# Kernel tuning notes

Hardware: AMD Instinct MI355X
Metric: run time of the kernel (lower is better)

Reference implementation:

```python
import jax, jax.numpy as jnp
import numpy as np
from jax.scipy.special import logsumexp

B, S, H, T, M = 64, 512, 768, 500, 8
POSITION_WEIGHT = 0.6
LABEL_SMOOTH = 0.1
GAMMA = 2.0


def setup_inputs() -> dict:
    key = jax.random.key(0)
    ks = jax.random.split(key, 12)
    hidden = jax.random.normal(ks[0], (B, S, H), jnp.float32)  # BERT sequence_output stand-in
    lengths = jax.random.randint(ks[1], (B,), S // 2, S + 1)
    attention_mask = (jnp.arange(S)[None, :] < lengths[:, None]).astype(jnp.int32)
    position_labels = jax.random.randint(ks[2], (B, S), 0, 3).astype(jnp.int32)
    type_labels = jax.random.randint(ks[3], (B, M), 0, T).astype(jnp.int32)
    starts = jax.random.randint(ks[4], (B, M), 1, S // 2)
    ends = starts + jax.random.randint(ks[5], (B, M), 2, 8)
    valid = jax.random.uniform(ks[6], (B, M)) < 0.8  # some (batch, span) slots unused, like the original sum()>0 filter
    target_positions = jnp.where(valid[..., None], jnp.stack([starts, ends], -1), 0).astype(jnp.int32)
    # CRF params exactly as hardcoded in __init__
    trans = jnp.array([[-5.0, 20.0, -10000.0], [-50.0, 0.0, 50.0], [0.0, -50.0, 30.0]], jnp.float32)
    start_trans = jnp.array([0.0, 0.0, -10000.0], jnp.float32)
    end_trans = jnp.array([0.0, -100.0, 0.0], jnp.float32)
    return {
        'hidden': hidden,
        'attention_mask': attention_mask,
        'position_labels': position_labels,
        'type_labels': type_labels,
        'target_positions': target_positions,
        'bi_label_weight': jnp.asarray(0.5, jnp.float32),
        'W_pos': 0.02 * jax.random.normal(ks[7], (H, 3), jnp.float32),
        'b_pos': jnp.zeros((3,), jnp.float32),
        'start_trans': start_trans,
        'end_trans': end_trans,
        'trans': trans,
        'att_W1': 0.02 * jax.random.normal(ks[8], (H, 64), jnp.float32),
        'att_b1': jnp.zeros((64,), jnp.float32),
        'att_W2': 0.02 * jax.random.normal(ks[9], (64, 1), jnp.float32),
        'att_b2': jnp.zeros((1,), jnp.float32),
        'W_type': 0.02 * jax.random.normal(ks[10], (H, T), jnp.float32),
        'b_type': jnp.zeros((T,), jnp.float32),
    }


def crf_nll(em, labels, mask, start_trans, end_trans, trans):
    # torchcrf-style masked negative log-likelihood, reduction='none'
    maskf = mask.astype(em.dtype)
    emit = jnp.take_along_axis(em, labels[..., None], -1)[..., 0]  # [B,S]
    emit_score = (emit * maskf).sum(1)
    tr = trans[labels[:, :-1], labels[:, 1:]]  # [B,S-1]
    tr_score = (tr * maskf[:, 1:]).sum(1)
    last = mask.sum(1) - 1
    last_tags = jnp.take_along_axis(labels, last[:, None], 1)[:, 0]
    score = start_trans[labels[:, 0]] + emit_score + tr_score + end_trans[last_tags]
    # log partition via scan over time
    alpha = start_trans[None, :] + em[:, 0]  # [B,3]
    def step(alpha, xs):
        em_t, m_t = xs
        nxt = logsumexp(alpha[:, :, None] + trans[None, :, :] + em_t[:, None, :], axis=1)
        return jnp.where(m_t[:, None], nxt, alpha), None
    alpha, _ = jax.lax.scan(step, alpha, (em[:, 1:].transpose(1, 0, 2), mask[:, 1:].T))
    logZ = logsumexp(alpha + end_trans[None, :], axis=-1)
    return logZ - score  # = -log_likelihood


def reference(hidden, attention_mask, position_labels, type_labels, target_positions,
              bi_label_weight, W_pos, b_pos, start_trans, end_trans, trans,
              att_W1, att_b1, att_W2, att_b2, W_type, b_type):
    mask = attention_mask.astype(bool)
    emissions = hidden @ W_pos + b_pos  # [B,S,3]
    w = jnp.where(position_labels > 0, 1.0 + bi_label_weight, 1.0)[..., None]
    em_w = emissions * w
    position_loss = crf_nll(em_w, position_labels, mask, start_trans, end_trans, trans).mean()

    # span attention pooling, batched over all (B,M) pairs instead of the Python loop
    scores = (jnp.tanh(hidden @ att_W1 + att_b1) @ att_W2 + att_b2)[..., 0]  # [B,S]
    starts = target_positions[..., 0]
    ends = target_positions[..., 1]
    valid = target_positions.sum(-1) > 0  # [B,M]
    pos = jnp.arange(hidden.shape[1])
    span_mask = (pos[None, None, :] >= starts[..., None]) & (pos[None, None, :] < ends[..., None])  # [B,M,S]
    att = jnp.where(span_mask, scores[:, None, :], -1e9)
    aw = jax.nn.softmax(att, axis=-1)  # per-span softmax == softmax over the gathered span
    pooled = jnp.einsum('bms,bsh->bmh', aw, hidden)  # [B,M,H]
    logits = pooled @ W_type + b_type  # [B,M,T]

    # label-smoothed focal loss over valid spans only
    nT = logits.shape[-1]
    onehot = jax.nn.one_hot(type_labels, nT, dtype=logits.dtype)
    smooth = onehot * (1.0 - LABEL_SMOOTH) + LABEL_SMOOTH / nT
    logp = jax.nn.log_softmax(logits, axis=-1)
    probs = jnp.exp(logp)
    ce = -(smooth * logp).sum(-1)
    pt = (smooth * probs).sum(-1)
    focal = ce * (1.0 - pt) ** GAMMA
    v = valid.astype(focal.dtype)
    type_loss = (focal * v).sum() / jnp.maximum(v.sum(), 1.0) * 10.0

    joint = POSITION_WEIGHT * position_loss + (1.0 - POSITION_WEIGHT) * type_loss
    return jnp.stack([joint, position_loss, type_loss])
```

## Files before the change

### kernel.cpp

```cpp
#include <hip/hip_runtime.h>

#define L2E 1.44269504088896340736f
#define LN2 0.69314718055994530942f
#define NEGB -1e30f

typedef float f32x4 __attribute__((ext_vector_type(4)));
typedef __bf16 bf16x8 __attribute__((ext_vector_type(8)));

static constexpr int NB = 64, NS = 512, NH = 768, NT = 500, NM = 8;

static constexpr size_t WT_ALL_OFF   = 0;
static constexpr size_t WT_TYPE_OFF  = 122880;
static constexpr size_t EM_T_OFF     = 909312;
static constexpr size_t SCORES_OFF   = 1302528;
static constexpr size_t LABELS_T_OFF = 1433600;
static constexpr size_t LEN_OFF      = 1564672;
static constexpr size_t SCAL_OFF     = 3399936;
static constexpr size_t MATM_OFF     = 3400192;
static constexpr size_t PSC_OFF      = 3547648;

__device__ __forceinline__ unsigned short f2bf(float f) {
  unsigned u = __builtin_bit_cast(unsigned, f);
  u += 0x7FFFu + ((u >> 16) & 1u);
  return (unsigned short)(u >> 16);
}
__device__ __forceinline__ float sel3(float a, float b, float c, int i) {
  return i == 0 ? a : (i == 1 ? b : c);
}
__device__ __forceinline__ float lse3(float x, float y, float z) {
  float m = fmaxf(fmaxf(x, y), z);
  float p = exp2f((x - m) * L2E) + exp2f((y - m) * L2E) + exp2f((z - m) * L2E);
  return m + log2f(p) * LN2;
}
__device__ __forceinline__ bf16x8 pack8(float4 lo, float4 hi) {
  union { unsigned u[4]; bf16x8 v; } r;
  asm("v_cvt_pk_bf16_f32 %0, %1, %2" : "=v"(r.u[0]) : "v"(lo.x), "v"(lo.y));
  asm("v_cvt_pk_bf16_f32 %0, %1, %2" : "=v"(r.u[1]) : "v"(lo.z), "v"(lo.w));
  asm("v_cvt_pk_bf16_f32 %0, %1, %2" : "=v"(r.u[2]) : "v"(hi.x), "v"(hi.y));
  asm("v_cvt_pk_bf16_f32 %0, %1, %2" : "=v"(r.u[3]) : "v"(hi.z), "v"(hi.w));
  return r.v;
}
__device__ __forceinline__ void gload_lds16(const void* g, void* l) {
  __builtin_amdgcn_global_load_lds(
      (const __attribute__((address_space(1))) unsigned*)g,
      (__attribute__((address_space(3))) unsigned*)l, 16, 0, 0);
}

__global__ __launch_bounds__(256) void ka_prep(
    const float* __restrict__ W1, const float* __restrict__ Wpos,
    const float* __restrict__ Wtype, const int* __restrict__ amask,
    unsigned short* __restrict__ wt_all, unsigned short* __restrict__ wt_type,
    int* __restrict__ lengths, float* __restrict__ scal) {
  const int bid = blockIdx.x, t = threadIdx.x;
  if (bid < 108) {
    __shared__ float tl[64][65];
    const bool is_type = bid < 96;
    const int kt = is_type ? (bid % 12) : (bid - 96);
    const int k0 = kt * 64;
    const int n0 = is_type ? (bid / 12) * 64 : 0;
    const int ld = is_type ? 500 : 64;
    const int nlim = is_type ? 500 : 64;
    const float* src = is_type ? Wtype : W1;
    unsigned short* dst = is_type ? wt_type : wt_all;
    const int n = t & 63;
    #pragma unroll
    for (int i = 0; i < 16; ++i) {
      int k = i * 4 + (t >> 6);
      tl[k][n] = (n0 + n < nlim) ? src[(size_t)(k0 + k) * ld + n0 + n] : 0.f;
    }
    __syncthreads();
    const int k = t & 63;
    #pragma unroll
    for (int i = 0; i < 16; ++i) {
      int nn = i * 4 + (t >> 6);
      dst[(size_t)(n0 + nn) * 768 + k0 + k] = f2bf(tl[k][nn]);
    }
  } else if (bid == 108) {
    for (int idx = t; idx < 16 * 768; idx += 256) {
      int n = 64 + idx / 768, k = idx % 768;
      float v = (n < 67) ? Wpos[k * 3 + (n - 64)] : 0.f;
      wt_all[(size_t)n * 768 + k] = f2bf(v);
    }
  } else {
    __shared__ int part[256];
    int bb = t >> 2, qq = t & 3;
    const int4* mp = (const int4*)(amask + bb * 512 + qq * 128);
    int s = 0;
    #pragma unroll 8
    for (int i = 0; i < 32; ++i) { int4 v = mp[i]; s += v.x + v.y + v.z + v.w; }
    part[t] = s;
    __syncthreads();
    if (qq == 0) lengths[bb] = part[t] + part[t + 1] + part[t + 2] + part[t + 3];
    if (t == 0) { scal[1] = 0.f; scal[2] = 0.f; scal[3] = 0.f; }
  }
}

__global__ __launch_bounds__(256) void k1_gemm(
    const float* __restrict__ hidden, const int* __restrict__ plab,
    const float* __restrict__ bpos, const float* __restrict__ b1,
    const float* __restrict__ W2, const float* __restrict__ b2,
    const float* __restrict__ biw, const unsigned short* __restrict__ wt_all,
    float* __restrict__ em_t, float* __restrict__ scores, int* __restrict__ labels_t) {
  __shared__ uint4 As[4][512];
  __shared__ uint4 Bs[4][512];
  const int t = threadIdx.x, w = t >> 6, l = t & 63;
  const int row0 = blockIdx.x * 64;
  const int c16 = l & 15, q = l >> 4;

  f32x4 acc[5];
  #pragma unroll
  for (int nt = 0; nt < 5; ++nt) acc[nt] = (f32x4){0.f, 0.f, 0.f, 0.f};

  auto stage = [&](int it) {
    const int bi = it & 3;
    const int k0 = it * 32;
    #pragma unroll
    for (int u = 0; u < 2; ++u) {
      int i = w * 128 + u * 64 + l;
      int row = i >> 3;
      int ss = (i & 7) ^ (row & 7);
      gload_lds16(hidden + (size_t)(row0 + row) * 768 + k0 + 4 * ss,
                  (void*)(As[bi] + (w * 128 + u * 64)));
    }
    #pragma unroll
    for (int u = 0; u < 2; ++u) {
      int i = w * 128 + u * 64 + l;
      int row = i >> 2;
      int ss = (i & 3) ^ ((row >> 1) & 3);
      gload_lds16(wt_all + (size_t)row * 768 + k0 + 8 * ss,
                  (void*)(Bs[bi] + (w * 128 + u * 64)));
    }
  };

  stage(0); stage(1);
  for (int it = 0; it < 24; ++it) {
    if (it < 22) stage(it + 2);
    if (it < 22)       asm volatile("s_waitcnt vmcnt(8)" ::: "memory");
    else if (it == 22) asm volatile("s_waitcnt vmcnt(4)" ::: "memory");
    else               asm volatile("s_waitcnt vmcnt(0)" ::: "memory");
    __builtin_amdgcn_s_barrier();
    __builtin_amdgcn_sched_barrier(0);

    const int bi = it & 3;
    const char* Ab = (const char*)As[bi];
    const char* Bb = (const char*)Bs[bi];
    const int arow = 16 * w + c16, r7 = arow & 7;
    float4 alo = *(const float4*)(Ab + arow * 128 + (((2 * q + 0) ^ r7) << 4));
    float4 ahi = *(const float4*)(Ab + arow * 128 + (((2 * q + 1) ^ r7) << 4));
    bf16x8 a = pack8(alo, ahi);
    #pragma unroll
    for (int nt = 0; nt < 5; ++nt) {
      const int brow = 16 * nt + c16;
      bf16x8 b = *(const bf16x8*)(Bb + brow * 64 + ((q ^ ((brow >> 1) & 3)) << 4));
      acc[nt] = __builtin_amdgcn_mfma_f32_16x16x32_bf16(a, b, acc[nt], 0, 0, 0);
    }
  }

  const float bias2 = b2[0];
  #pragma unroll
  for (int r = 0; r < 4; ++r) {
    float s = 0.f;
    #pragma unroll
    for (int nt = 0; nt < 4; ++nt) {
      int c = 16 * nt + c16;
      float x = acc[nt][r] + b1[c];
      float th = 1.f - 2.f / (1.f + exp2f(x * (2.f * L2E)));
      s += th * W2[c];
    }
    #pragma unroll
    for (int off = 1; off < 16; off <<= 1) s += __shfl_xor(s, off, 64);
    if (c16 == 0) {
      int row = row0 + 16 * w + 4 * q + r;
      scores[row] = s + bias2;
    }
  }
  if (c16 < 3) {
    const float bi = biw[0];
    #pragma unroll
    for (int r = 0; r < 4; ++r) {
      int row = row0 + 16 * w + 4 * q + r;
      int bb = row >> 9, ss = row & 511;
      int lab = plab[row];
      float wgt = (lab > 0) ? 1.f + bi : 1.f;
      float ev = (acc[4][r] + bpos[c16]) * wgt;
      em_t[(ss * 3 + c16) * 64 + bb] = ev;
      if (c16 == 0) labels_t[ss * 64 + bb] = lab;
    }
  }
}

__global__ __launch_bounds__(256) void kf_fused(
    const float* __restrict__ hidden, const float* __restrict__ scores,
    const int* __restrict__ tpos, const int* __restrict__ tlab,
    const unsigned short* __restrict__ wt_type, const float* __restrict__ btype,
    const float* __restrict__ em_t, const int* __restrict__ labels_t,
    const int* __restrict__ lengths, const float* __restrict__ trans,
    const float* __restrict__ strans, const float* __restrict__ etrans,
    float* __restrict__ matM, float* __restrict__ psc, float* __restrict__ scal,
    float* __restrict__ out) {
  __shared__ unsigned short Apool[8][776];
  __shared__ uint4 Bt[8][512];
  __shared__ float logitsL[8][516];
  __shared__ float fRow[8], vRow[8];
  __shared__ int last_flag;
  const int bid = blockIdx.x;
  const int t = threadIdx.x, w = t >> 6, l = t & 63;

  if (bid >= 64) {
    const int b = l, c = (bid - 64) * 4 + w;
    float T0 = trans[0], T1 = trans[1], T2 = trans[2];
    float T3 = trans[3], T4 = trans[4], T5 = trans[5];
    float T6 = trans[6], T7 = trans[7], T8 = trans[8];
    const int L = lengths[b];
    const int s0 = 8 * c;
    int labp = labels_t[(c ? (s0 - 1) : 0) * 64 + b];

    float E0[8], E1[8], E2[8]; int LB[8];
    #pragma unroll
    for (int i = 0; i < 8; ++i) {
      E0[i] = em_t[((s0 + i) * 3 + 0) * 64 + b];
      E1[i] = em_t[((s0 + i) * 3 + 1) * 64 + b];
      E2[i] = em_t[((s0 + i) * 3 + 2) * 64 + b];
      LB[i] = labels_t[(s0 + i) * 64 + b];
    }

    float M[9];
    #pragma unroll
    for (int i = 0; i < 9; ++i) M[i] = (i == 0 || i == 4 || i == 8) ? 0.f : NEGB;
    float sc = 0.f;

    #pragma unroll
    for (int i = 0; i < 8; ++i) {
      int s = s0 + i;
      bool act = (s >= 1) && (s < L);
      float N[9];
      #pragma unroll
      for (int r = 0; r < 3; ++r) {
        float ma = M[3 * r], mb = M[3 * r + 1], mc = M[3 * r + 2];
        N[3 * r + 0] = lse3(ma + T0, mb + T3, mc + T6) + E0[i];
        N[3 * r + 1] = lse3(ma + T1, mb + T4, mc + T7) + E1[i];
        N[3 * r + 2] = lse3(ma + T2, mb + T5, mc + T8) + E2[i];
      }
      #pragma unroll
      for (int r = 0; r < 9; ++r) M[r] = act ? N[r] : M[r];
      int lab = LB[i];
      float ev = sel3(E0[i], E1[i], E2[i], lab);
      float trv = sel3(sel3(T0, T1, T2, lab),
                       sel3(T3, T4, T5, lab),
                       sel3(T6, T7, T8, lab), labp);
      sc += act ? (ev + trv) : 0.f;
      labp = lab;
    }
    #pragma unroll
    for (int i = 0; i < 9; ++i) matM[(c * 9 + i) * 64 + b] = M[i];
    psc[c * 64 + b] = sc;
  } else {
    const int b = bid;
    {
      const int sp = t >> 5;
      const int span = b * 8 + sp;
      const int st = tpos[span * 2], en = tpos[span * 2 + 1];
      const int len = (st + en > 0) ? (en - st) : 0;
      float sv[7], aw[7];
      float wm = -1e30f;
      #pragma unroll
      for (int j = 0; j < 7; ++j) {
        sv[j] = (j < len) ? scores[b * 512 + st + j] : -1e30f;
        wm = fmaxf(wm, sv[j]);
      }
      float den = 0.f;
      #pragma unroll
      for (int j = 0; j < 7; ++j) {
        aw[j] = (j < len) ? exp2f((sv[j] - wm) * L2E) : 0.f;
        den += aw[j];
      }
      float inv = (den > 0.f) ? 1.f / den : 0.f;
      #pragma unroll
      for (int j = 0; j < 7; ++j) aw[j] *= inv;

      const int h0 = (t & 31) * 24;
      float ap[24];
      #pragma unroll
      for (int i = 0; i < 24; ++i) ap[i] = 0.f;
      #pragma unroll
      for (int j = 0; j < 7; ++j) {
        if (j < len) {
          const float4* hp = (const float4*)(hidden + (size_t)(b * 512 + st + j) * 768 + h0);
          #pragma unroll
          for (int i = 0; i < 6; ++i) {
            float4 v = hp[i];
            ap[4 * i + 0] += aw[j] * v.x; ap[4 * i + 1] += aw[j] * v.y;
            ap[4 * i + 2] += aw[j] * v.z; ap[4 * i + 3] += aw[j] * v.w;
          }
        }
      }
      unsigned short* dp = &Apool[sp][h0];
      #pragma unroll
      for (int g = 0; g < 3; ++g) {
        uint4 v;
        v.x = (unsigned)f2bf(ap[8 * g + 0]) | ((unsigned)f2bf(ap[8 * g + 1]) << 16);
        v.y = (unsigned)f2bf(ap[8 * g + 2]) | ((unsigned)f2bf(ap[8 * g + 3]) << 16);
        v.z = (unsigned)f2bf(ap[8 * g + 4]) | ((unsigned)f2bf(ap[8 * g + 5]) << 16);
        v.w = (unsigned)f2bf(ap[8 * g + 6]) | ((unsigned)f2bf(ap[8 * g + 7]) << 16);
        *(uint4*)(dp + 8 * g) = v;
      }
    }
    __syncthreads();

    auto stageB = [&](int bi, int ct, int kt) {
      #pragma unroll
      for (int u = 0; u < 2; ++u) {
        int i = u * 256 + t;
        int row = i >> 3;
        int ss = (i & 7) ^ (row & 7);
        gload_lds16(wt_type + (size_t)(ct * 64 + row) * 768 + kt * 64 + 8 * ss,
                    (void*)(Bt[bi] + i));
      }
    };
    const int c16 = l & 15, q = l >> 4;
    const bf16x8 zerov = (bf16x8)(__bf16)0.f;
    #pragma unroll
    for (int s0 = 0; s0 < 6; ++s0) stageB(s0, 0, s0);

    int step = 0;
    for (int ct = 0; ct < 8; ++ct) {
      f32x4 acc = (f32x4){0.f, 0.f, 0.f, 0.f};
      for (int kt = 0; kt < 12; ++kt, ++step) {
        if (step < 90) {
          int ns = step + 6;
          stageB(ns & 7, ns / 12, ns % 12);
          asm volatile("s_waitcnt vmcnt(12)" ::: "memory");
        }
        else if (step == 90) asm volatile("s_waitcnt vmcnt(10)" ::: "memory");
        else if (step == 91) asm volatile("s_waitcnt vmcnt(8)" ::: "memory");
        else if (step == 92) asm volatile("s_waitcnt vmcnt(6)" ::: "memory");
        else if (step == 93) asm volatile("s_waitcnt vmcnt(4)" ::: "memory");
        else if (step == 94) asm volatile("s_waitcnt vmcnt(2)" ::: "memory");
        else                 asm volatile("s_waitcnt vmcnt(0)" ::: "memory");
        __builtin_amdgcn_s_barrier();
        __builtin_amdgcn_sched_barrier(0);

        const char* Bb = (const char*)Bt[step & 7];
        const int brow = w * 16 + c16, r7 = brow & 7;
        bf16x8 a0 = (c16 < 8) ? *(const bf16x8*)(&Apool[c16][kt * 64 + q * 8]) : zerov;
        bf16x8 a1 = (c16 < 8) ? *(const bf16x8*)(&Apool[c16][kt * 64 + 32 + q * 8]) : zerov;
        bf16x8 b0 = *(const bf16x8*)(Bb + brow * 128 + (((0 + q) ^ r7) << 4));
        bf16x8 b1 = *(const bf16x8*)(Bb + brow * 128 + (((4 + q) ^ r7) << 4));
        acc = __builtin_amdgcn_mfma_f32_16x16x32_bf16(a0, b0, acc, 0, 0, 0);
        acc = __builtin_amdgcn_mfma_f32_16x16x32_bf16(a1, b1, acc, 0, 0, 0);
      }
      if (q < 2) {
        #pragma unroll
        for (int r = 0; r < 4; ++r)
          logitsL[4 * q + r][ct * 64 + w * 16 + c16] = acc[r];
      }
    }
    __syncthreads();

    #pragma unroll
    for (int rr = 0; rr < 2; ++rr) {
      const int row = 2 * w + rr;
      float v[8];
      #pragma unroll
      for (int j = 0; j < 8; ++j) {
        int col = l + 64 * j;
        v[j] = (col < 500) ? logitsL[row][col] + btype[col] : -1e30f;
      }
      float m = v[0];
      #pragma unroll
      for (int j = 1; j < 8; ++j) m = fmaxf(m, v[j]);
      #pragma unroll
      for (int off = 1; off < 64; off <<= 1) m = fmaxf(m, __shfl_xor(m, off, 64));
      float p = 0.f, slog = 0.f;
      #pragma unroll
      for (int j = 0; j < 8; ++j) {
        p += exp2f((v[j] - m) * L2E);
        slog += (l + 64 * j < 500) ? v[j] : 0.f;
      }
      #pragma unroll
      for (int off = 1; off < 64; off <<= 1) {
        p += __shfl_xor(p, off, 64);
        slog += __shfl_xor(slog, off, 64);
      }
      float logZ = m + log2f(p) * LN2;
      int lbl = tlab[b * 8 + row];
      float vlv = logitsL[row][lbl] + btype[lbl];
      float lp = vlv - logZ;
      float ce = -(0.9f * lp + 2e-4f * (slog - 500.f * logZ));
      float pt = 0.9f * exp2f(lp * L2E) + 2e-4f;
      float focal = ce * (1.f - pt) * (1.f - pt);
      int span = b * 8 + row;
      bool valid = (tpos[span * 2] + tpos[span * 2 + 1]) > 0;
      if (l == 0) {
        fRow[row] = valid ? focal : 0.f;
        vRow[row] = valid ? 1.f : 0.f;
      }
    }
    __syncthreads();
    if (t == 0) {
      float fv = 0.f, vv = 0.f;
      #pragma unroll
      for (int i = 0; i < 8; ++i) { fv += fRow[i]; vv += vRow[i]; }
      atomicAdd(&scal[1], fv);
      atomicAdd(&scal[2], vv);
    }
  }

  __syncthreads();
  if (t == 0) {
    __threadfence();
    unsigned old = atomicAdd((unsigned*)&scal[3], 1u);
    last_flag = (old == 79u);
  }
  __syncthreads();
  if (last_flag && t < 64) {
    __threadfence();
    const int b = t;
    const int L = lengths[b];
    const float st0 = strans[0], st1 = strans[1], st2 = strans[2];
    const float et0 = etrans[0], et1 = etrans[1], et2 = etrans[2];
    float e00 = em_t[0 * 64 + b], e01 = em_t[1 * 64 + b], e02 = em_t[2 * 64 + b];
    int lab0 = labels_t[b];
    float a0 = st0 + e00, a1 = st1 + e01, a2 = st2 + e02;
    float score = sel3(st0, st1, st2, lab0) + sel3(e00, e01, e02, lab0);

    float cur[4][10];
    #pragma unroll
    for (int j = 0; j < 4; ++j) {
      #pragma unroll
      for (int i = 0; i < 9; ++i) cur[j][i] = matM[(j * 9 + i) * 64 + b];
      cur[j][9] = psc[j * 64 + b];
    }
    for (int r = 0; r < 16; ++r) {
      float nxt[4][10];
      if (r < 15) {
        #pragma unroll
        for (int j = 0; j < 4; ++j) {
          int c = (r + 1) * 4 + j;
          #pragma unroll
          for (int i = 0; i < 9; ++i) nxt[j][i] = matM[(c * 9 + i) * 64 + b];
          nxt[j][9] = psc[c * 64 + b];
        }
      }
      #pragma unroll
      for (int j = 0; j < 4; ++j) {
        float n0 = lse3(a0 + cur[j][0], a1 + cur[j][3], a2 + cur[j][6]);
        float n1 = lse3(a0 + cur[j][1], a1 + cur[j][4], a2 + cur[j][7]);
        float n2 = lse3(a0 + cur[j][2], a1 + cur[j][5], a2 + cur[j][8]);
        a0 = n0; a1 = n1; a2 = n2;
        score += cur[j][9];
      }
      if (r < 15) {
        #pragma unroll
        for (int j = 0; j < 4; ++j)
          #pragma unroll
          for (int i = 0; i < 10; ++i) cur[j][i] = nxt[j][i];
      }
    }
    int last = labels_t[(L - 1) * 64 + b];
    score += sel3(et0, et1, et2, last);
    float logZ = lse3(a0 + et0, a1 + et1, a2 + et2);
    float nll = logZ - score;
    #pragma unroll
    for (int off = 1; off < 64; off <<= 1) nll += __shfl_xor(nll, off, 64);
    if (b == 0) {
      float pos = nll / 64.f;
      float type = scal[1] / fmaxf(scal[2], 1.f) * 10.f;
      out[0] = 0.6f * pos + 0.4f * type;
      out[1] = pos;
      out[2] = type;
    }
  }
}

extern "C" void kernel_launch(void* const* d_in, const int* in_sizes, int n_in,
                              void* d_out, int out_size, void* d_ws, size_t ws_size,
                              hipStream_t stream) {
  const float* hidden = (const float*)d_in[0];
  const int*   amask  = (const int*)d_in[1];
  const int*   plab   = (const int*)d_in[2];
  const int*   tlab   = (const int*)d_in[3];
  const int*   tpos   = (const int*)d_in[4];
  const float* biw    = (const float*)d_in[5];
  const float* Wpos   = (const float*)d_in[6];
  const float* bpos   = (const float*)d_in[7];
  const float* strans = (const float*)d_in[8];
  const float* etrans = (const float*)d_in[9];
  const float* trans  = (const float*)d_in[10];
  const float* W1     = (const float*)d_in[11];
  const float* b1     = (const float*)d_in[12];
  const float* W2     = (const float*)d_in[13];
  const float* b2     = (const float*)d_in[14];
  const float* Wtype  = (const float*)d_in[15];
  const float* btype  = (const float*)d_in[16];
  float* out = (float*)d_out;
  char* ws = (char*)d_ws;

  unsigned short* wt_all  = (unsigned short*)(ws + WT_ALL_OFF);
  unsigned short* wt_type = (unsigned short*)(ws + WT_TYPE_OFF);
  float* em_t    = (float*)(ws + EM_T_OFF);
  float* scores  = (float*)(ws + SCORES_OFF);
  int*   labelsT = (int*)(ws + LABELS_T_OFF);
  int*   lengths = (int*)(ws + LEN_OFF);
  float* scal    = (float*)(ws + SCAL_OFF);
  float* matM    = (float*)(ws + MATM_OFF);
  float* psc     = (float*)(ws + PSC_OFF);

  ka_prep<<<110, 256, 0, stream>>>(W1, Wpos, Wtype, amask, wt_all, wt_type, lengths, scal);
  k1_gemm<<<512, 256, 0, stream>>>(hidden, plab, bpos, b1, W2, b2, biw, wt_all,
                                   em_t, scores, labelsT);
  kf_fused<<<80, 256, 0, stream>>>(hidden, scores, tpos, tlab, wt_type, btype,
                                   em_t, labelsT, lengths, trans, strans, etrans,
                                   matM, psc, scal, out);
}
```

Before: 98.06 us.

## Split fused tail kernel into separate CRF-chunk, pooling, type-GEMM and final kernels

```diff
diff --git a/kernel.cpp b/kernel.cpp
--- a/kernel.cpp
+++ b/kernel.cpp
@@ -15,6 +15,7 @@
 static constexpr size_t SCORES_OFF   = 1302528;
 static constexpr size_t LABELS_T_OFF = 1433600;
 static constexpr size_t LEN_OFF      = 1564672;
+static constexpr size_t POOLED_OFF   = 2351360;
 static constexpr size_t SCAL_OFF     = 3399936;
 static constexpr size_t MATM_OFF     = 3400192;
 static constexpr size_t PSC_OFF      = 3547648;
@@ -189,287 +190,258 @@
   }
 }
 
-__global__ __launch_bounds__(256) void kf_fused(
-    const float* __restrict__ hidden, const float* __restrict__ scores,
-    const int* __restrict__ tpos, const int* __restrict__ tlab,
-    const unsigned short* __restrict__ wt_type, const float* __restrict__ btype,
+__global__ __launch_bounds__(64) void k2a_chunk(
     const float* __restrict__ em_t, const int* __restrict__ labels_t,
     const int* __restrict__ lengths, const float* __restrict__ trans,
-    const float* __restrict__ strans, const float* __restrict__ etrans,
-    float* __restrict__ matM, float* __restrict__ psc, float* __restrict__ scal,
-    float* __restrict__ out) {
+    float* __restrict__ matM, float* __restrict__ psc) {
+  const int b = threadIdx.x, c = blockIdx.x;
+  float T0 = trans[0], T1 = trans[1], T2 = trans[2];
+  float T3 = trans[3], T4 = trans[4], T5 = trans[5];
+  float T6 = trans[6], T7 = trans[7], T8 = trans[8];
+  const int L = lengths[b];
+  const int s0 = 8 * c;
+  int labp = labels_t[(c ? (s0 - 1) : 0) * 64 + b];
+
+  float E0[8], E1[8], E2[8]; int LB[8];
+  #pragma unroll
+  for (int i = 0; i < 8; ++i) {
+    E0[i] = em_t[((s0 + i) * 3 + 0) * 64 + b];
+    E1[i] = em_t[((s0 + i) * 3 + 1) * 64 + b];
+    E2[i] = em_t[((s0 + i) * 3 + 2) * 64 + b];
+    LB[i] = labels_t[(s0 + i) * 64 + b];
+  }
+
+  float M[9];
+  #pragma unroll
+  for (int i = 0; i < 9; ++i) M[i] = (i == 0 || i == 4 || i == 8) ? 0.f : NEGB;
+  float sc = 0.f;
+
+  #pragma unroll
+  for (int i = 0; i < 8; ++i) {
+    int s = s0 + i;
+    bool act = (s >= 1) && (s < L);
+    float N[9];
+    #pragma unroll
+    for (int r = 0; r < 3; ++r) {
+      float ma = M[3 * r], mb = M[3 * r + 1], mc = M[3 * r + 2];
+      N[3 * r + 0] = lse3(ma + T0, mb + T3, mc + T6) + E0[i];
+      N[3 * r + 1] = lse3(ma + T1, mb + T4, mc + T7) + E1[i];
+      N[3 * r + 2] = lse3(ma + T2, mb + T5, mc + T8) + E2[i];
+    }
+    #pragma unroll
+    for (int r = 0; r < 9; ++r) M[r] = act ? N[r] : M[r];
+    int lab = LB[i];
+    float ev = sel3(E0[i], E1[i], E2[i], lab);
+    float trv = sel3(sel3(T0, T1, T2, lab),
+                     sel3(T3, T4, T5, lab),
+                     sel3(T6, T7, T8, lab), labp);
+    sc += act ? (ev + trv) : 0.f;
+    labp = lab;
+  }
+  #pragma unroll
+  for (int i = 0; i < 9; ++i) matM[(c * 9 + i) * 64 + b] = M[i];
+  psc[c * 64 + b] = sc;
+}
+
+__global__ __launch_bounds__(64) void k_pool(
+    const float* __restrict__ hidden, const float* __restrict__ scores,
+    const int* __restrict__ tpos, unsigned short* __restrict__ pooled) {
+  const int span = blockIdx.x, l = threadIdx.x;
+  const int b = span >> 3;
+  const int st = tpos[span * 2], en = tpos[span * 2 + 1];
+  int len = (st + en > 0) ? (en - st) : 0;
+  float sv[7], aw[7];
+  float wm = -1e30f;
+  #pragma unroll
+  for (int j = 0; j < 7; ++j) {
+    sv[j] = (j < len) ? scores[b * 512 + st + j] : -1e30f;
+    wm = fmaxf(wm, sv[j]);
+  }
+  float den = 0.f;
+  #pragma unroll
+  for (int j = 0; j < 7; ++j) {
+    aw[j] = (j < len) ? exp2f((sv[j] - wm) * L2E) : 0.f;
+    den += aw[j];
+  }
+  float inv = (den > 0.f) ? 1.f / den : 0.f;
+  #pragma unroll
+  for (int j = 0; j < 7; ++j) aw[j] *= inv;
+  #pragma unroll
+  for (int r = 0; r < 12; ++r) {
+    int h = l + 64 * r;
+    float acc = 0.f;
+    #pragma unroll
+    for (int j = 0; j < 7; ++j)
+      if (j < len) acc += aw[j] * hidden[(size_t)(b * 512 + st + j) * 768 + h];
+    pooled[span * 768 + h] = f2bf(acc);
+  }
+}
+
+__global__ __launch_bounds__(512) void k_tg(
+    const unsigned short* __restrict__ pooled, const unsigned short* __restrict__ wt_type,
+    const float* __restrict__ btype, const int* __restrict__ tlab,
+    const int* __restrict__ tpos, float* __restrict__ scal) {
   __shared__ unsigned short Apool[8][776];
-  __shared__ uint4 Bt[8][512];
   __shared__ float logitsL[8][516];
   __shared__ float fRow[8], vRow[8];
-  __shared__ int last_flag;
-  const int bid = blockIdx.x;
   const int t = threadIdx.x, w = t >> 6, l = t & 63;
-
-  if (bid >= 64) {
-    const int b = l, c = (bid - 64) * 4 + w;
-    float T0 = trans[0], T1 = trans[1], T2 = trans[2];
-    float T3 = trans[3], T4 = trans[4], T5 = trans[5];
-    float T6 = trans[6], T7 = trans[7], T8 = trans[8];
-    const int L = lengths[b];
-    const int s0 = 8 * c;
-    int labp = labels_t[(c ? (s0 - 1) : 0) * 64 + b];
-
-    float E0[8], E1[8], E2[8]; int LB[8];
-    #pragma unroll
-    for (int i = 0; i < 8; ++i) {
-      E0[i] = em_t[((s0 + i) * 3 + 0) * 64 + b];
-      E1[i] = em_t[((s0 + i) * 3 + 1) * 64 + b];
-      E2[i] = em_t[((s0 + i) * 3 + 2) * 64 + b];
-      LB[i] = labels_t[(s0 + i) * 64 + b];
-    }
-
-    float M[9];
-    #pragma unroll
-    for (int i = 0; i < 9; ++i) M[i] = (i == 0 || i == 4 || i == 8) ? 0.f : NEGB;
-    float sc = 0.f;
-
-    #pragma unroll
-    for (int i = 0; i < 8; ++i) {
-      int s = s0 + i;
-      bool act = (s >= 1) && (s < L);
-      float N[9];
+  const int b = blockIdx.x;
+  const int c16 = l & 15, q = l >> 4;
+
+  #pragma unroll
+  for (int u = 0; u < 2; ++u) {
+    int idx = t + 512 * u;
+    if (idx < 768) {
+      int row = idx / 96, c8 = idx % 96;
+      *(uint4*)(&Apool[row][c8 * 8]) = *(const uint4*)(pooled + (size_t)(b * 8 + row) * 768 + c8 * 8);
+    }
+  }
+  __syncthreads();
+
+  f32x4 acc[4];
+  #pragma unroll
+  for (int nt = 0; nt < 4; ++nt) acc[nt] = (f32x4){0.f, 0.f, 0.f, 0.f};
+  const bf16x8 zerov = (bf16x8)(__bf16)0.f;
+  const unsigned short* bp[4];
+  #pragma unroll
+  for (int nt = 0; nt < 4; ++nt)
+    bp[nt] = wt_type + (size_t)(64 * w + 16 * nt + c16) * 768 + 8 * q;
+
+  bf16x8 bcur[4], bnxt[4];
+  #pragma unroll
+  for (int nt = 0; nt < 4; ++nt) bcur[nt] = *(const bf16x8*)(bp[nt]);
+  for (int ks = 0; ks < 24; ++ks) {
+    if (ks < 23) {
       #pragma unroll
-      for (int r = 0; r < 3; ++r) {
-        float ma = M[3 * r], mb = M[3 * r + 1], mc = M[3 * r + 2];
-        N[3 * r + 0] = lse3(ma + T0, mb + T3, mc + T6) + E0[i];
-        N[3 * r + 1] = lse3(ma + T1, mb + T4, mc + T7) + E1[i];
-        N[3 * r + 2] = lse3(ma + T2, mb + T5, mc + T8) + E2[i];
-      }
+      for (int nt = 0; nt < 4; ++nt) bnxt[nt] = *(const bf16x8*)(bp[nt] + (ks + 1) * 32);
+    }
+    bf16x8 a = (c16 < 8) ? *(const bf16x8*)(&Apool[c16][ks * 32 + 8 * q]) : zerov;
+    #pragma unroll
+    for (int nt = 0; nt < 4; ++nt)
+      acc[nt] = __builtin_amdgcn_mfma_f32_16x16x32_bf16(a, bcur[nt], acc[nt], 0, 0, 0);
+    #pragma unroll
+    for (int nt = 0; nt < 4; ++nt) bcur[nt] = bnxt[nt];
+  }
+  if (q < 2) {
+    #pragma unroll
+    for (int nt = 0; nt < 4; ++nt) {
       #pragma unroll
-      for (int r = 0; r < 9; ++r) M[r] = act ? N[r] : M[r];
-      int lab = LB[i];
-      float ev = sel3(E0[i], E1[i], E2[i], lab);
-      float trv = sel3(sel3(T0, T1, T2, lab),
-                       sel3(T3, T4, T5, lab),
-                       sel3(T6, T7, T8, lab), labp);
-      sc += act ? (ev + trv) : 0.f;
-      labp = lab;
-    }
-    #pragma unroll
-    for (int i = 0; i < 9; ++i) matM[(c * 9 + i) * 64 + b] = M[i];
-    psc[c * 64 + b] = sc;
-  } else {
-    const int b = bid;
-    {
-      const int sp = t >> 5;
-      const int span = b * 8 + sp;
-      const int st = tpos[span * 2], en = tpos[span * 2 + 1];
-      const int len = (st + en > 0) ? (en - st) : 0;
-      float sv[7], aw[7];
-      float wm = -1e30f;
-      #pragma unroll
-      for (int j = 0; j < 7; ++j) {
-        sv[j] = (j < len) ? scores[b * 512 + st + j] : -1e30f;
-        wm = fmaxf(wm, sv[j]);
-      }
-      float den = 0.f;
-      #pragma unroll
-      for (int j = 0; j < 7; ++j) {
-        aw[j] = (j < len) ? exp2f((sv[j] - wm) * L2E) : 0.f;
-        den += aw[j];
-      }
-      float inv = (den > 0.f) ? 1.f / den : 0.f;
-      #pragma unroll
-      for (int j = 0; j < 7; ++j) aw[j] *= inv;
-
-      const int h0 = (t & 31) * 24;
-      float ap[24];
-      #pragma unroll
-      for (int i = 0; i < 24; ++i) ap[i] = 0.f;
-      #pragma unroll
-      for (int j = 0; j < 7; ++j) {
-        if (j < len) {
-          const float4* hp = (const float4*)(hidden + (size_t)(b * 512 + st + j) * 768 + h0);
-          #pragma unroll
-          for (int i = 0; i < 6; ++i) {
-            float4 v = hp[i];
-            ap[4 * i + 0] += aw[j] * v.x; ap[4 * i + 1] += aw[j] * v.y;
-            ap[4 * i + 2] += aw[j] * v.z; ap[4 * i + 3] += aw[j] * v.w;
-          }
-        }
-      }
-      unsigned short* dp = &Apool[sp][h0];
-      #pragma unroll
-      for (int g = 0; g < 3; ++g) {
-        uint4 v;
-        v.x = (unsigned)f2bf(ap[8 * g + 0]) | ((unsigned)f2bf(ap[8 * g + 1]) << 16);
-        v.y = (unsigned)f2bf(ap[8 * g + 2]) | ((unsigned)f2bf(ap[8 * g + 3]) << 16);
-        v.z = (unsigned)f2bf(ap[8 * g + 4]) | ((unsigned)f2bf(ap[8 * g + 5]) << 16);
-        v.w = (unsigned)f2bf(ap[8 * g + 6]) | ((unsigned)f2bf(ap[8 * g + 7]) << 16);
-        *(uint4*)(dp + 8 * g) = v;
-      }
-    }
-    __syncthreads();
-
-    auto stageB = [&](int bi, int ct, int kt) {
-      #pragma unroll
-      for (int u = 0; u < 2; ++u) {
-        int i = u * 256 + t;
-        int row = i >> 3;
-        int ss = (i & 7) ^ (row & 7);
-        gload_lds16(wt_type + (size_t)(ct * 64 + row) * 768 + kt * 64 + 8 * ss,
-                    (void*)(Bt[bi] + i));
-      }
-    };
-    const int c16 = l & 15, q = l >> 4;
-    const bf16x8 zerov = (bf16x8)(__bf16)0.f;
-    #pragma unroll
-    for (int s0 = 0; s0 < 6; ++s0) stageB(s0, 0, s0);
-
-    int step = 0;
-    for (int ct = 0; ct < 8; ++ct) {
-      f32x4 acc = (f32x4){0.f, 0.f, 0.f, 0.f};
-      for (int kt = 0; kt < 12; ++kt, ++step) {
-        if (step < 90) {
-          int ns = step + 6;
-          stageB(ns & 7, ns / 12, ns % 12);
-          asm volatile("s_waitcnt vmcnt(12)" ::: "memory");
-        }
-        else if (step == 90) asm volatile("s_waitcnt vmcnt(10)" ::: "memory");
-        else if (step == 91) asm volatile("s_waitcnt vmcnt(8)" ::: "memory");
-        else if (step == 92) asm volatile("s_waitcnt vmcnt(6)" ::: "memory");
-        else if (step == 93) asm volatile("s_waitcnt vmcnt(4)" ::: "memory");
-        else if (step == 94) asm volatile("s_waitcnt vmcnt(2)" ::: "memory");
-        else                 asm volatile("s_waitcnt vmcnt(0)" ::: "memory");
-        __builtin_amdgcn_s_barrier();
-        __builtin_amdgcn_sched_barrier(0);
-
-        const char* Bb = (const char*)Bt[step & 7];
-        const int brow = w * 16 + c16, r7 = brow & 7;
-        bf16x8 a0 = (c16 < 8) ? *(const bf16x8*)(&Apool[c16][kt * 64 + q * 8]) : zerov;
-        bf16x8 a1 = (c16 < 8) ? *(const bf16x8*)(&Apool[c16][kt * 64 + 32 + q * 8]) : zerov;
-        bf16x8 b0 = *(const bf16x8*)(Bb + brow * 128 + (((0 + q) ^ r7) << 4));
-        bf16x8 b1 = *(const bf16x8*)(Bb + brow * 128 + (((4 + q) ^ r7) << 4));
-        acc = __builtin_amdgcn_mfma_f32_16x16x32_bf16(a0, b0, acc, 0, 0, 0);
-        acc = __builtin_amdgcn_mfma_f32_16x16x32_bf16(a1, b1, acc, 0, 0, 0);
-      }
-      if (q < 2) {
-        #pragma unroll
-        for (int r = 0; r < 4; ++r)
-          logitsL[4 * q + r][ct * 64 + w * 16 + c16] = acc[r];
-      }
-    }
-    __syncthreads();
-
-    #pragma unroll
-    for (int rr = 0; rr < 2; ++rr) {
-      const int row = 2 * w + rr;
-      float v[8];
-      #pragma unroll
-      for (int j = 0; j < 8; ++j) {
-        int col = l + 64 * j;
-        v[j] = (col < 500) ? logitsL[row][col] + btype[col] : -1e30f;
-      }
-      float m = v[0];
-      #pragma unroll
-      for (int j = 1; j < 8; ++j) m = fmaxf(m, v[j]);
-      #pragma unroll
-      for (int off = 1; off < 64; off <<= 1) m = fmaxf(m, __shfl_xor(m, off, 64));
-      float p = 0.f, slog = 0.f;
-      #pragma unroll
-      for (int j = 0; j < 8; ++j) {
-        p += exp2f((v[j] - m) * L2E);
-        slog += (l + 64 * j < 500) ? v[j] : 0.f;
-      }
-      #pragma unroll
-      for (int off = 1; off < 64; off <<= 1) {
-        p += __shfl_xor(p, off, 64);
-        slog += __shfl_xor(slog, off, 64);
-      }
-      float logZ = m + log2f(p) * LN2;
-      int lbl = tlab[b * 8 + row];
-      float vlv = logitsL[row][lbl] + btype[lbl];
-      float lp = vlv - logZ;
-      float ce = -(0.9f * lp + 2e-4f * (slog - 500.f * logZ));
-      float pt = 0.9f * exp2f(lp * L2E) + 2e-4f;
-      float focal = ce * (1.f - pt) * (1.f - pt);
-      int span = b * 8 + row;
-      bool valid = (tpos[span * 2] + tpos[span * 2 + 1]) > 0;
-      if (l == 0) {
-        fRow[row] = valid ? focal : 0.f;
-        vRow[row] = valid ? 1.f : 0.f;
-      }
-    }
-    __syncthreads();
-    if (t == 0) {
-      float fv = 0.f, vv = 0.f;
-      #pragma unroll
-      for (int i = 0; i < 8; ++i) { fv += fRow[i]; vv += vRow[i]; }
-      atomicAdd(&scal[1], fv);
-      atomicAdd(&scal[2], vv);
-    }
-  }
-
+      for (int r = 0; r < 4; ++r)
+        logitsL[4 * q + r][64 * w + 16 * nt + c16] = acc[nt][r];
+    }
+  }
+  __syncthreads();
+
+  {
+    const int row = w;
+    float v[8];
+    #pragma unroll
+    for (int j = 0; j < 8; ++j) {
+      int col = l + 64 * j;
+      v[j] = (col < 500) ? logitsL[row][col] + btype[col] : -1e30f;
+    }
+    float m = v[0];
+    #pragma unroll
+    for (int j = 1; j < 8; ++j) m = fmaxf(m, v[j]);
+    #pragma unroll
+    for (int off = 1; off < 64; off <<= 1) m = fmaxf(m, __shfl_xor(m, off, 64));
+    float p = 0.f, slog = 0.f;
+    #pragma unroll
+    for (int j = 0; j < 8; ++j) {
+      p += exp2f((v[j] - m) * L2E);
+      slog += (l + 64 * j < 500) ? v[j] : 0.f;
+    }
+    #pragma unroll
+    for (int off = 1; off < 64; off <<= 1) {
+      p += __shfl_xor(p, off, 64);
+      slog += __shfl_xor(slog, off, 64);
+    }
+    float logZ = m + log2f(p) * LN2;
+    int lbl = tlab[b * 8 + row];
+    float vlv = logitsL[row][lbl] + btype[lbl];
+    float lp = vlv - logZ;
+    float ce = -(0.9f * lp + 2e-4f * (slog - 500.f * logZ));
+    float pt = 0.9f * exp2f(lp * L2E) + 2e-4f;
+    float focal = ce * (1.f - pt) * (1.f - pt);
+    int span = b * 8 + row;
+    bool valid = (tpos[span * 2] + tpos[span * 2 + 1]) > 0;
+    if (l == 0) {
+      fRow[row] = valid ? focal : 0.f;
+      vRow[row] = valid ? 1.f : 0.f;
+    }
+  }
   __syncthreads();
   if (t == 0) {
-    __threadfence();
-    unsigned old = atomicAdd((unsigned*)&scal[3], 1u);
-    last_flag = (old == 79u);
-  }
-  __syncthreads();
-  if (last_flag && t < 64) {
-    __threadfence();
-    const int b = t;
-    const int L = lengths[b];
-    const float st0 = strans[0], st1 = strans[1], st2 = strans[2];
-    const float et0 = etrans[0], et1 = etrans[1], et2 = etrans[2];
-    float e00 = em_t[0 * 64 + b], e01 = em_t[1 * 64 + b], e02 = em_t[2 * 64 + b];
-    int lab0 = labels_t[b];
-    float a0 = st0 + e00, a1 = st1 + e01, a2 = st2 + e02;
-    float score = sel3(st0, st1, st2, lab0) + sel3(e00, e01, e02, lab0);
-
-    float cur[4][10];
-    #pragma unroll
-    for (int j = 0; j < 4; ++j) {
-      #pragma unroll
-      for (int i = 0; i < 9; ++i) cur[j][i] = matM[(j * 9 + i) * 64 + b];
-      cur[j][9] = psc[j * 64 + b];
-    }
-    for (int r = 0; r < 16; ++r) {
-      float nxt[4][10];
-      if (r < 15) {
-        #pragma unroll
-        for (int j = 0; j < 4; ++j) {
-          int c = (r + 1) * 4 + j;
-          #pragma unroll
-          for (int i = 0; i < 9; ++i) nxt[j][i] = matM[(c * 9 + i) * 64 + b];
-          nxt[j][9] = psc[c * 64 + b];
-        }
-      }
+    float fv = 0.f, vv = 0.f;
+    #pragma unroll
+    for (int i = 0; i < 8; ++i) { fv += fRow[i]; vv += vRow[i]; }
+    atomicAdd(&scal[1], fv);
+    atomicAdd(&scal[2], vv);
+  }
+}
+
+__global__ __launch_bounds__(64) void k_final(
+    const float* __restrict__ em_t, const int* __restrict__ labels_t,
+    const int* __restrict__ lengths, const float* __restrict__ strans,
+    const float* __restrict__ etrans, const float* __restrict__ matM,
+    const float* __restrict__ psc, const float* __restrict__ scal,
+    float* __restrict__ out) {
+  const int b = threadIdx.x;
+  const int L = lengths[b];
+  const float st0 = strans[0], st1 = strans[1], st2 = strans[2];
+  const float et0 = etrans[0], et1 = etrans[1], et2 = etrans[2];
+  float e00 = em_t[0 * 64 + b], e01 = em_t[1 * 64 + b], e02 = em_t[2 * 64 + b];
+  int lab0 = labels_t[b];
+  float a0 = st0 + e00, a1 = st1 + e01, a2 = st2 + e02;
+  float score = sel3(st0, st1, st2, lab0) + sel3(e00, e01, e02, lab0);
+
+  float cur[4][10];
+  #pragma unroll
+  for (int j = 0; j < 4; ++j) {
+    #pragma unroll
+    for (int i = 0; i < 9; ++i) cur[j][i] = matM[(j * 9 + i) * 64 + b];
+    cur[j][9] = psc[j * 64 + b];
+  }
+
+  for (int r = 0; r < 16; ++r) {
+    float nxt[4][10];
+    if (r < 15) {
       #pragma unroll
       for (int j = 0; j < 4; ++j) {
-        float n0 = lse3(a0 + cur[j][0], a1 + cur[j][3], a2 + cur[j][6]);
-        float n1 = lse3(a0 + cur[j][1], a1 + cur[j][4], a2 + cur[j][7]);
-        float n2 = lse3(a0 + cur[j][2], a1 + cur[j][5], a2 + cur[j][8]);
-        a0 = n0; a1 = n1; a2 = n2;
-        score += cur[j][9];
+        int c = (r + 1) * 4 + j;
+        #pragma unroll
+        for (int i = 0; i < 9; ++i) nxt[j][i] = matM[(c * 9 + i) * 64 + b];
+        nxt[j][9] = psc[c * 64 + b];
       }
-      if (r < 15) {
+    }
+    #pragma unroll
+    for (int j = 0; j < 4; ++j) {
+      float n0 = lse3(a0 + cur[j][0], a1 + cur[j][3], a2 + cur[j][6]);
+      float n1 = lse3(a0 + cur[j][1], a1 + cur[j][4], a2 + cur[j][7]);
+      float n2 = lse3(a0 + cur[j][2], a1 + cur[j][5], a2 + cur[j][8]);
+      a0 = n0; a1 = n1; a2 = n2;
+      score += cur[j][9];
+    }
+    if (r < 15) {
+      #pragma unroll
+      for (int j = 0; j < 4; ++j)
         #pragma unroll
-        for (int j = 0; j < 4; ++j)
-          #pragma unroll
-          for (int i = 0; i < 10; ++i) cur[j][i] = nxt[j][i];
-      }
-    }
-    int last = labels_t[(L - 1) * 64 + b];
-    score += sel3(et0, et1, et2, last);
-    float logZ = lse3(a0 + et0, a1 + et1, a2 + et2);
-    float nll = logZ - score;
-    #pragma unroll
-    for (int off = 1; off < 64; off <<= 1) nll += __shfl_xor(nll, off, 64);
-    if (b == 0) {
-      float pos = nll / 64.f;
-      float type = scal[1] / fmaxf(scal[2], 1.f) * 10.f;
-      out[0] = 0.6f * pos + 0.4f * type;
-      out[1] = pos;
-      out[2] = type;
-    }
+        for (int i = 0; i < 10; ++i) cur[j][i] = nxt[j][i];
+    }
+  }
+
+  int last = labels_t[(L - 1) * 64 + b];
+  score += sel3(et0, et1, et2, last);
+  float logZ = lse3(a0 + et0, a1 + et1, a2 + et2);
+  float nll = logZ - score;
+  #pragma unroll
+  for (int off = 1; off < 64; off <<= 1) nll += __shfl_xor(nll, off, 64);
+  if (b == 0) {
+    float pos = nll / 64.f;
+    float type = scal[1] / fmaxf(scal[2], 1.f) * 10.f;
+    out[0] = 0.6f * pos + 0.4f * type;
+    out[1] = pos;
+    out[2] = type;
   }
 }
 
@@ -502,6 +474,7 @@
   float* scores  = (float*)(ws + SCORES_OFF);
   int*   labelsT = (int*)(ws + LABELS_T_OFF);
   int*   lengths = (int*)(ws + LEN_OFF);
+  unsigned short* pooled = (unsigned short*)(ws + POOLED_OFF);
   float* scal    = (float*)(ws + SCAL_OFF);
   float* matM    = (float*)(ws + MATM_OFF);
   float* psc     = (float*)(ws + PSC_OFF);
@@ -509,7 +482,8 @@
   ka_prep<<<110, 256, 0, stream>>>(W1, Wpos, Wtype, amask, wt_all, wt_type, lengths, scal);
   k1_gemm<<<512, 256, 0, stream>>>(hidden, plab, bpos, b1, W2, b2, biw, wt_all,
                                    em_t, scores, labelsT);
-  kf_fused<<<80, 256, 0, stream>>>(hidden, scores, tpos, tlab, wt_type, btype,
-                                   em_t, labelsT, lengths, trans, strans, etrans,
-                                   matM, psc, scal, out);
-}
+  k2a_chunk<<<64, 64, 0, stream>>>(em_t, labelsT, lengths, trans, matM, psc);
+  k_pool<<<512, 64, 0, stream>>>(hidden, scores, tpos, pooled);
+  k_tg<<<64, 512, 0, stream>>>(pooled, wt_type, btype, tlab, tpos, scal);
+  k_final<<<1, 64, 0, stream>>>(em_t, labelsT, lengths, strans, etrans, matM, psc, scal, out);
+}
```

Result: slower. 108.9 us (+11.1%).
